# Kernel optimization log

Measured on AMD Instinct MI355X. Metric: run time of the kernel, lower is better.

## Reference

```python
import jax, jax.numpy as jnp
import numpy as np

K = 32  # neighbors per query point


def _gather_points(x, idx):
    # x: [B, N, D], idx: [B, M, k] -> [B, M, k, D]
    B, M, k = idx.shape
    D = x.shape[-1]
    flat = jnp.take_along_axis(x, idx.reshape(B, M * k, 1), axis=1)
    return flat.reshape(B, M, k, D)


def setup_inputs() -> dict:
    key = jax.random.key(0)
    k1, k2, k3, k4, k5 = jax.random.split(key, 5)
    B, N, M, Cin = 16, 4096, 1024, 64
    pos = jax.random.normal(k1, (B, N, 3), dtype=jnp.float32)
    features = jax.random.normal(k2, (B, N, Cin), dtype=jnp.float32)
    idx = jax.random.randint(k3, (B, M), 0, N, dtype=jnp.int64)
    # 1x1 conv2d MLP params: (Cin+3) -> 64 -> 128 (use_xyz adds 3 channels)
    W1 = jax.random.normal(k4, (Cin + 3, 64), dtype=jnp.float32) * (1.0 / np.sqrt(Cin + 3))
    b1 = jnp.zeros((64,), dtype=jnp.float32)
    W2 = jax.random.normal(k5, (64, 128), dtype=jnp.float32) * (1.0 / np.sqrt(64))
    b2 = jnp.zeros((128,), dtype=jnp.float32)
    return {"pos": pos, "features": features, "W1": W1, "b1": b1,
            "W2": W2, "b2": b2, "idx": idx}


def reference(pos, features, W1, b1, W2, b2, idx):
    # pos: [B,N,3], features: [B,N,C], idx: [B,M] query-point indices
    pos_q = jnp.take_along_axis(pos, idx[..., None], axis=1)  # [B,M,3]
    # squared-distance knn: [B,M,N]
    d2 = (jnp.sum(pos_q ** 2, -1, keepdims=True)
          + jnp.sum(pos ** 2, -1)[:, None, :]
          - 2.0 * jnp.einsum("bmd,bnd->bmn", pos_q, pos))
    _, nn_idx = jax.lax.top_k(-d2, K)  # [B,M,K] nearest neighbors
    grouped_pos = _gather_points(pos, nn_idx)          # [B,M,K,3]
    grouped_feat = _gather_points(features, nn_idx)    # [B,M,K,C]
    rel = grouped_pos - pos_q[:, :, None, :]           # recenter groups
    x = jnp.concatenate([rel, grouped_feat], axis=-1)  # [B,M,K,C+3] (use_xyz)
    # 1x1 conv2d MLP == per-point linear + ReLU on channel dim
    h = jax.nn.relu(jnp.einsum("bmkc,cd->bmkd", x, W1) + b1)
    h = jax.nn.relu(jnp.einsum("bmkc,cd->bmkd", h, W2) + b2)
    out = jnp.max(h, axis=-2)  # max over K neighbors -> [B,M,128]
    return (pos_q, out)
```

## Files before the change

### kernel.cpp

```cpp
#include <hip/hip_runtime.h>

#define NPTS  4096
#define MQ    1024
#define BATCH 16
#define KNN   32
#define CIN   64
#define H1D   64
#define H2D   128

typedef _Float16 half8 __attribute__((ext_vector_type(8)));
typedef float    floatx4 __attribute__((ext_vector_type(4)));

#define WS_NN_BYTES ((size_t)BATCH * MQ * KNN * 4)
#define W1F_HALVES  (3 * 4 * 64 * 8)
#define W2F_HALVES  (2 * 8 * 64 * 8)
#define WS_P4_OFF   (WS_NN_BYTES + (W1F_HALVES + W2F_HALVES) * 2)
#define WS_X16_OFF  (WS_P4_OFF + (size_t)BATCH * NPTS * 16)
#define XROW        96

__global__ __launch_bounds__(256) void wprep_kernel(
    const float* __restrict__ W1, const float* __restrict__ W2,
    const float* __restrict__ pos, const float* __restrict__ feat,
    _Float16* __restrict__ wout, float4* __restrict__ pos4,
    _Float16* __restrict__ x16)
{
    const int gid = blockIdx.x * 256 + threadIdx.x;
    if (gid < 768) {
        const int s = gid;
        const int kc = s >> 8, nt = (s >> 6) & 3, lane = s & 63;
        const int col = lane & 15, quad = lane >> 4;
        half8 ph;
#pragma unroll
        for (int j = 0; j < 8; ++j) {
            const int k = kc * 32 + quad * 8 + j;
            ph[j] = (k < 67) ? (_Float16)W1[k * H1D + nt * 16 + col] : (_Float16)0.0f;
        }
        *(half8*)(wout + (size_t)s * 8) = ph;
    } else if (gid < 1792) {
        const int s2 = gid - 768;
        const int kc2 = s2 >> 9, nt2 = (s2 >> 6) & 7, lane = s2 & 63;
        const int col = lane & 15, quad = lane >> 4;
        half8 ph;
#pragma unroll
        for (int j = 0; j < 8; ++j) {
            const int k = kc2 * 32 + quad * 8 + j;
            ph[j] = (_Float16)W2[k * H2D + nt2 * 16 + col];
        }
        *(half8*)(wout + (size_t)W1F_HALVES + (size_t)s2 * 8) = ph;
    } else if (gid < 1792 + BATCH * NPTS) {
        const int p = gid - 1792;
        const float px = pos[p * 3 + 0], py = pos[p * 3 + 1], pz = pos[p * 3 + 2];
        float4 v;
        v.x = px; v.y = py; v.z = pz;
        v.w = __fadd_rn(__fadd_rn(__fmul_rn(px, px), __fmul_rn(py, py)),
                        __fmul_rn(pz, pz));
        pos4[p] = v;
    } else {
        const int p2 = gid - (1792 + BATCH * NPTS);
        if (p2 < BATCH * NPTS * 12) {
            const int p  = p2 / 12;
            const int ci = p2 - p * 12;
            const float* fr = feat + (size_t)p * CIN;
            half8 ph;
#pragma unroll
            for (int jj = 0; jj < 8; ++jj) {
                const int c = ci * 8 + jj - 3;
                const float v2 = (c >= 0 && c < CIN) ? fr[c] : 0.0f;
                ph[jj] = (_Float16)v2;
            }
            *(half8*)(x16 + (size_t)p * XROW + ci * 8) = ph;
        }
    }
}

__global__ __launch_bounds__(256, 4) void knn_kernel(
    const float4* __restrict__ pos4, const int* __restrict__ idx,
    float* __restrict__ pos_q, int* __restrict__ nn)
{
    const int bid = blockIdx.x;
    const int b   = bid >> 10;
    const int m   = bid & (MQ - 1);
    const int t   = threadIdx.x;
    const int wv  = t >> 6, lane = t & 63;

    __shared__ __align__(16) unsigned int hist[1024];
    __shared__ unsigned int wred[8];
    __shared__ unsigned int wsum[4];
    __shared__ unsigned int sc[8];
    __shared__ unsigned int ckey[64];
    __shared__ int          cidx[64];
    __shared__ int          outidx[KNN];

    const float4* pb4 = pos4 + (size_t)b * NPTS;
    const int qn = idx[(size_t)b * MQ + m];
    const float4 qv = pb4[qn];
    const float qq = qv.w;

    *(uint4*)&hist[t * 4] = make_uint4(0u, 0u, 0u, 0u);

    float4 p[16];
#pragma unroll
    for (int i = 0; i < 16; ++i) p[i] = pb4[i * 256 + t];

    unsigned int k[16];
    unsigned int lmin = 0xFFFFFFFFu, lmax = 0u;
#pragma unroll
    for (int i = 0; i < 16; ++i) {
        const float qp = __fadd_rn(__fadd_rn(__fmul_rn(qv.x, p[i].x), __fmul_rn(qv.y, p[i].y)),
                                   __fmul_rn(qv.z, p[i].z));
        const float d2 = __fsub_rn(__fadd_rn(qq, p[i].w), __fmul_rn(2.0f, qp));
        unsigned int u = __float_as_uint(d2);
        u = (u & 0x80000000u) ? ~u : (u | 0x80000000u);
        k[i] = u;
        lmin = min(lmin, u);
        lmax = max(lmax, u);
    }
#pragma unroll
    for (int off = 32; off; off >>= 1) {
        lmin = min(lmin, (unsigned int)__shfl_xor(lmin, off));
        lmax = max(lmax, (unsigned int)__shfl_xor(lmax, off));
    }
    if (lane == 0) { wred[wv] = lmin; wred[4 + wv] = lmax; }
    __syncthreads();
    const unsigned int umin = min(min(wred[0], wred[1]), min(wred[2], wred[3]));
    const unsigned int umax = max(max(wred[4], wred[5]), max(wred[6], wred[7]));
    const unsigned int rng  = umax - umin;
#pragma unroll
    for (int i = 0; i < 16; ++i) k[i] -= umin;

    int sCur;
    {
        const int bits = (rng == 0u) ? 0 : (32 - __clz(rng));
        sCur = (bits > 10) ? (bits - 10) : 0;
    }

#pragma unroll
    for (int i = 0; i < 16; ++i) atomicAdd(&hist[k[i] >> sCur], 1u);
    __syncthreads();

    unsigned int prefix = 0u, rank = KNN - 1;
    int bcnt = 0, nb = 0;
    bool first = true;
    for (;;) {
        const uint4 c4 = *(const uint4*)&hist[t * 4];
        const unsigned int ssum = c4.x + c4.y + c4.z + c4.w;
        unsigned int v = ssum;
#pragma unroll
        for (int off = 1; off < 64; off <<= 1) {
            const unsigned int o = __shfl_up(v, off);
            if (lane >= off) v += o;
        }
        if (lane == 63) wsum[wv] = v;
        __syncthreads();
        unsigned int woff = 0;
        for (int i = 0; i < wv; ++i) woff += wsum[i];
        const unsigned int incl = woff + v, excl = incl - ssum;
        if (rank >= excl && rank < incl) {
            const unsigned int cnt[4] = {c4.x, c4.y, c4.z, c4.w};
            unsigned int e = excl;
            for (int j = 0; j < 4; ++j) {
                if (rank < e + cnt[j]) {
                    sc[0] = (unsigned int)(t * 4 + j);
                    sc[1] = rank - e;
                    sc[2] = cnt[j];
                    break;
                }
                e += cnt[j];
            }
        }
        __syncthreads();
        const unsigned int bin = sc[0];
        rank = sc[1];
        bcnt = (int)sc[2];
        prefix = first ? bin : ((prefix << nb) | bin);
        first = false;
        if (bcnt <= 64 || sCur == 0) break;

        const int sNext = (sCur > 10) ? (sCur - 10) : 0;
        nb = sCur - sNext;
        __syncthreads();
        *(uint4*)&hist[t * 4] = make_uint4(0u, 0u, 0u, 0u);
        __syncthreads();
        const unsigned int mask = (1u << nb) - 1u;
#pragma unroll
        for (int i = 0; i < 16; ++i) {
            if ((k[i] >> sCur) == prefix)
                atomicAdd(&hist[(k[i] >> sNext) & mask], 1u);
        }
        __syncthreads();
        sCur = sNext;
    }

    if (t == 0) { sc[3] = 0u; sc[4] = 0u; }
    __syncthreads();
#pragma unroll
    for (int i = 0; i < 16; ++i) {
        const unsigned int hp = k[i] >> sCur;
        if (hp < prefix) {
            outidx[atomicAdd(&sc[3], 1u)] = i * 256 + t;
        } else if (hp == prefix) {
            const unsigned int slot = atomicAdd(&sc[4], 1u);
            if (slot < 64u) { ckey[slot] = k[i]; cidx[slot] = i * 256 + t; }
        }
    }
    __syncthreads();
    const int defcnt  = (int)sc[3];
    const int candcnt = min((int)sc[4], 64);

    if (wv == 0) {
        const unsigned int k_l = (lane < candcnt) ? ckey[lane] : 0xFFFFFFFFu;
        const int          i_l = (lane < candcnt) ? cidx[lane] : 0x7FFFFFFF;
        int rk = 0;
        for (int j = 0; j < candcnt; ++j) {
            const unsigned int kj = __shfl(k_l, j);
            const int          ij = __shfl(i_l, j);
            if (kj < k_l || (kj == k_l && ij < i_l)) ++rk;
        }
        if (lane < candcnt && rk <= (int)rank) outidx[defcnt + rk] = i_l;
    }
    __syncthreads();
    if (t < KNN) nn[(size_t)bid * KNN + t] = outidx[t];
    if (t == 0) {
        pos_q[(size_t)bid * 3 + 0] = qv.x;
        pos_q[(size_t)bid * 3 + 1] = qv.y;
        pos_q[(size_t)bid * 3 + 2] = qv.z;
    }
}

__global__ __launch_bounds__(256, 6) void mlp_kernel(
    const float4* __restrict__ pos4, const _Float16* __restrict__ x16,
    const float* __restrict__ b1, const float* __restrict__ b2,
    const float* __restrict__ pos_q, const int* __restrict__ nn,
    const _Float16* __restrict__ wf, float* __restrict__ out)
{
    __shared__ _Float16 sh[4 * 2048];
    const int t = threadIdx.x;
    const int w = t >> 6, lane = t & 63;
    const int col = lane & 15, quad = lane >> 4;
    const int q = blockIdx.x * 4 + w;
    const int b = q >> 10;
    const int wbase = w * 2048;
    const int row = lane & 15;

    const int n0 = nn[(size_t)q * KNN + row];
    const int n1 = nn[(size_t)q * KNN + 16 + row];

    const _Float16* xb = x16 + (size_t)b * NPTS * XROW;
    const _Float16* x0 = xb + (size_t)n0 * XROW + quad * 8;
    const _Float16* x1 = xb + (size_t)n1 * XROW + quad * 8;

    half8 af[3][2];
    af[0][0] = *(const half8*)(x0);
    af[1][0] = *(const half8*)(x0 + 32);
    af[2][0] = *(const half8*)(x0 + 64);
    af[0][1] = *(const half8*)(x1);
    af[1][1] = *(const half8*)(x1 + 32);
    af[2][1] = *(const half8*)(x1 + 64);

    {
        const float qx = pos_q[(size_t)q * 3 + 0];
        const float qy = pos_q[(size_t)q * 3 + 1];
        const float qz = pos_q[(size_t)q * 3 + 2];
        const float4 pv0 = pos4[(size_t)b * NPTS + n0];
        const float4 pv1 = pos4[(size_t)b * NPTS + n1];
        if (quad == 0) {
            af[0][0][0] = (_Float16)(pv0.x - qx);
            af[0][0][1] = (_Float16)(pv0.y - qy);
            af[0][0][2] = (_Float16)(pv0.z - qz);
            af[0][1][0] = (_Float16)(pv1.x - qx);
            af[0][1][1] = (_Float16)(pv1.y - qy);
            af[0][1][2] = (_Float16)(pv1.z - qz);
        }
    }

#pragma unroll
    for (int nt = 0; nt < 4; ++nt) {
        const float bv = b1[nt * 16 + col];
        floatx4 acc0 = {bv, bv, bv, bv}, acc1 = acc0;
#pragma unroll
        for (int kc = 0; kc < 3; ++kc) {
            const half8 wb = *(const half8*)(wf + (size_t)((kc * 4 + nt) * 64 + lane) * 8);
            acc0 = __builtin_amdgcn_mfma_f32_16x16x32_f16(af[kc][0], wb, acc0, 0, 0, 0);
            acc1 = __builtin_amdgcn_mfma_f32_16x16x32_f16(af[kc][1], wb, acc1, 0, 0, 0);
        }
        const int kc2 = nt >> 1;
        const int quad2 = (((nt & 1) * 16) + col) >> 3;
        const int j2 = col & 7;
#pragma unroll
        for (int mt = 0; mt < 2; ++mt) {
            const floatx4 a = mt ? acc1 : acc0;
#pragma unroll
            for (int reg = 0; reg < 4; ++reg) {
                const int hrow = quad * 4 + reg;
                sh[wbase + ((kc2 * 2 + mt) * 64 + quad2 * 16 + hrow) * 8 + j2] =
                    (_Float16)fmaxf(a[reg], 0.0f);
            }
        }
    }

    half8 a2[2][2];
#pragma unroll
    for (int kc2 = 0; kc2 < 2; ++kc2)
#pragma unroll
        for (int mt = 0; mt < 2; ++mt)
            a2[kc2][mt] = *(const half8*)&sh[wbase + ((kc2 * 2 + mt) * 64 + lane) * 8];

    float* oq = out + (size_t)q * H2D;
#pragma unroll
    for (int nt2 = 0; nt2 < 8; ++nt2) {
        const float bv = b2[nt2 * 16 + col];
        floatx4 acc0 = {bv, bv, bv, bv}, acc1 = acc0;
#pragma unroll
        for (int kc2 = 0; kc2 < 2; ++kc2) {
            const half8 wb = *(const half8*)(wf + (size_t)W1F_HALVES
                                             + (size_t)((kc2 * 8 + nt2) * 64 + lane) * 8);
            acc0 = __builtin_amdgcn_mfma_f32_16x16x32_f16(a2[kc2][0], wb, acc0, 0, 0, 0);
            acc1 = __builtin_amdgcn_mfma_f32_16x16x32_f16(a2[kc2][1], wb, acc1, 0, 0, 0);
        }
        float mm = fmaxf(fmaxf(fmaxf(acc0[0], acc0[1]), fmaxf(acc0[2], acc0[3])),
                         fmaxf(fmaxf(acc1[0], acc1[1]), fmaxf(acc1[2], acc1[3])));
        mm = fmaxf(mm, 0.0f);
        mm = fmaxf(mm, __shfl_xor(mm, 16));
        mm = fmaxf(mm, __shfl_xor(mm, 32));
        if (lane < 16) oq[nt2 * 16 + lane] = mm;
    }
}

extern "C" void kernel_launch(void* const* d_in, const int* in_sizes, int n_in,
                              void* d_out, int out_size, void* d_ws, size_t ws_size,
                              hipStream_t stream)
{
    const float* pos  = (const float*)d_in[0];
    const float* feat = (const float*)d_in[1];
    const float* W1   = (const float*)d_in[2];
    const float* b1   = (const float*)d_in[3];
    const float* W2   = (const float*)d_in[4];
    const float* b2   = (const float*)d_in[5];
    const int*   idx  = (const int*)d_in[6];

    float* pos_q = (float*)d_out;
    float* out   = (float*)d_out + (size_t)BATCH * MQ * 3;
    int*       nn  = (int*)d_ws;
    _Float16*  wf  = (_Float16*)((char*)d_ws + WS_NN_BYTES);
    float4*    p4  = (float4*)((char*)d_ws + WS_P4_OFF);
    _Float16*  x16 = (_Float16*)((char*)d_ws + WS_X16_OFF);

    const int prep_threads = 1792 + BATCH * NPTS + BATCH * NPTS * 12;
    wprep_kernel<<<(prep_threads + 255) / 256, 256, 0, stream>>>(W1, W2, pos, feat,
                                                                 wf, p4, x16);
    knn_kernel<<<BATCH * MQ, 256, 0, stream>>>(p4, idx, pos_q, nn);
    mlp_kernel<<<BATCH * MQ / 4, 256, 0, stream>>>(p4, x16, b1, b2,
                                                   pos_q, nn, wf, out);
}
```

Baseline: 192.6 us.

## Fuse kNN selection and grouped MLP into one per-query kernel

Merges the kNN kernel and the MLP kernel so that each query's block selects its 32 neighbors and then runs the two MFMA layers itself. The four waves split the output column tiles of the MLP, exchanging the first-layer activations through shared memory. This removes the neighbor-index round trip through global memory, the pos_q reload and one kernel launch. In exchange the MLP now runs at the kNN kernel's occupancy, adds block-wide barriers, and each wave redundantly gathers the same neighbor rows.

```diff
diff --git a/kernel.cpp b/kernel.cpp
--- a/kernel.cpp
+++ b/kernel.cpp
@@ -73,9 +73,12 @@
     }
 }
 
-__global__ __launch_bounds__(256, 4) void knn_kernel(
-    const float4* __restrict__ pos4, const int* __restrict__ idx,
-    float* __restrict__ pos_q, int* __restrict__ nn)
+__global__ __launch_bounds__(256, 4) void pc_kernel(
+    const float4* __restrict__ pos4, const _Float16* __restrict__ x16,
+    const int* __restrict__ idx,
+    const float* __restrict__ b1, const float* __restrict__ b2,
+    const _Float16* __restrict__ wf,
+    float* __restrict__ pos_q, float* __restrict__ out)
 {
     const int bid = blockIdx.x;
     const int b   = bid >> 10;
@@ -90,6 +93,7 @@
     __shared__ unsigned int ckey[64];
     __shared__ int          cidx[64];
     __shared__ int          outidx[KNN];
+    __shared__ _Float16     sh[2048];
 
     const float4* pb4 = pos4 + (size_t)b * NPTS;
     const int qn = idx[(size_t)b * MQ + m];
@@ -218,32 +222,17 @@
         }
         if (lane < candcnt && rk <= (int)rank) outidx[defcnt + rk] = i_l;
     }
-    __syncthreads();
-    if (t < KNN) nn[(size_t)bid * KNN + t] = outidx[t];
     if (t == 0) {
         pos_q[(size_t)bid * 3 + 0] = qv.x;
         pos_q[(size_t)bid * 3 + 1] = qv.y;
         pos_q[(size_t)bid * 3 + 2] = qv.z;
     }
-}
-
-__global__ __launch_bounds__(256, 6) void mlp_kernel(
-    const float4* __restrict__ pos4, const _Float16* __restrict__ x16,
-    const float* __restrict__ b1, const float* __restrict__ b2,
-    const float* __restrict__ pos_q, const int* __restrict__ nn,
-    const _Float16* __restrict__ wf, float* __restrict__ out)
-{
-    __shared__ _Float16 sh[4 * 2048];
-    const int t = threadIdx.x;
-    const int w = t >> 6, lane = t & 63;
+    __syncthreads();
+
     const int col = lane & 15, quad = lane >> 4;
-    const int q = blockIdx.x * 4 + w;
-    const int b = q >> 10;
-    const int wbase = w * 2048;
-    const int row = lane & 15;
-
-    const int n0 = nn[(size_t)q * KNN + row];
-    const int n1 = nn[(size_t)q * KNN + 16 + row];
+
+    const int n0 = outidx[col];
+    const int n1 = outidx[16 + col];
 
     const _Float16* xb = x16 + (size_t)b * NPTS * XROW;
     const _Float16* x0 = xb + (size_t)n0 * XROW + quad * 8;
@@ -258,23 +247,20 @@
     af[2][1] = *(const half8*)(x1 + 64);
 
     {
-        const float qx = pos_q[(size_t)q * 3 + 0];
-        const float qy = pos_q[(size_t)q * 3 + 1];
-        const float qz = pos_q[(size_t)q * 3 + 2];
-        const float4 pv0 = pos4[(size_t)b * NPTS + n0];
-        const float4 pv1 = pos4[(size_t)b * NPTS + n1];
+        const float4 pv0 = pb4[n0];
+        const float4 pv1 = pb4[n1];
         if (quad == 0) {
-            af[0][0][0] = (_Float16)(pv0.x - qx);
-            af[0][0][1] = (_Float16)(pv0.y - qy);
-            af[0][0][2] = (_Float16)(pv0.z - qz);
-            af[0][1][0] = (_Float16)(pv1.x - qx);
-            af[0][1][1] = (_Float16)(pv1.y - qy);
-            af[0][1][2] = (_Float16)(pv1.z - qz);
-        }
-    }
-
-#pragma unroll
-    for (int nt = 0; nt < 4; ++nt) {
+            af[0][0][0] = (_Float16)(pv0.x - qv.x);
+            af[0][0][1] = (_Float16)(pv0.y - qv.y);
+            af[0][0][2] = (_Float16)(pv0.z - qv.z);
+            af[0][1][0] = (_Float16)(pv1.x - qv.x);
+            af[0][1][1] = (_Float16)(pv1.y - qv.y);
+            af[0][1][2] = (_Float16)(pv1.z - qv.z);
+        }
+    }
+
+    {
+        const int nt = wv;
         const float bv = b1[nt * 16 + col];
         floatx4 acc0 = {bv, bv, bv, bv}, acc1 = acc0;
 #pragma unroll
@@ -292,22 +278,24 @@
 #pragma unroll
             for (int reg = 0; reg < 4; ++reg) {
                 const int hrow = quad * 4 + reg;
-                sh[wbase + ((kc2 * 2 + mt) * 64 + quad2 * 16 + hrow) * 8 + j2] =
+                sh[((kc2 * 2 + mt) * 64 + quad2 * 16 + hrow) * 8 + j2] =
                     (_Float16)fmaxf(a[reg], 0.0f);
             }
         }
     }
+    __syncthreads();
 
     half8 a2[2][2];
 #pragma unroll
     for (int kc2 = 0; kc2 < 2; ++kc2)
 #pragma unroll
         for (int mt = 0; mt < 2; ++mt)
-            a2[kc2][mt] = *(const half8*)&sh[wbase + ((kc2 * 2 + mt) * 64 + lane) * 8];
-
-    float* oq = out + (size_t)q * H2D;
-#pragma unroll
-    for (int nt2 = 0; nt2 < 8; ++nt2) {
+            a2[kc2][mt] = *(const half8*)&sh[((kc2 * 2 + mt) * 64 + lane) * 8];
+
+    float* oq = out + (size_t)bid * H2D;
+#pragma unroll
+    for (int h = 0; h < 2; ++h) {
+        const int nt2 = wv * 2 + h;
         const float bv = b2[nt2 * 16 + col];
         floatx4 acc0 = {bv, bv, bv, bv}, acc1 = acc0;
 #pragma unroll
@@ -340,7 +328,6 @@
 
     float* pos_q = (float*)d_out;
     float* out   = (float*)d_out + (size_t)BATCH * MQ * 3;
-    int*       nn  = (int*)d_ws;
     _Float16*  wf  = (_Float16*)((char*)d_ws + WS_NN_BYTES);
     float4*    p4  = (float4*)((char*)d_ws + WS_P4_OFF);
     _Float16*  x16 = (_Float16*)((char*)d_ws + WS_X16_OFF);
@@ -348,7 +335,6 @@
     const int prep_threads = 1792 + BATCH * NPTS + BATCH * NPTS * 12;
     wprep_kernel<<<(prep_threads + 255) / 256, 256, 0, stream>>>(W1, W2, pos, feat,
                                                                  wf, p4, x16);
-    knn_kernel<<<BATCH * MQ, 256, 0, stream>>>(p4, idx, pos_q, nn);
-    mlp_kernel<<<BATCH * MQ / 4, 256, 0, stream>>>(p4, x16, b1, b2,
-                                                   pos_q, nn, wf, out);
+    pc_kernel<<<BATCH * MQ, 256, 0, stream>>>(p4, x16, idx, b1, b2, wf,
+                                              pos_q, out);
 }
```

Result: slower. 200.5 us (+4.1%).
